# Kernel optimization log

Measured on AMD Instinct MI355X. Metric: run time of the kernel, lower is better.

The kernel has to match this reference:

```python
import jax, jax.numpy as jnp
import numpy as np

B, N, D_MODEL, H = 2, 2048, 1024, 16
Q_CHUNK, K_CHUNK = 512, 1024
LN_EPS = 1e-5


def layer_norm(x, g, b):
    mu = x.mean(-1, keepdims=True)
    var = ((x - mu) ** 2).mean(-1, keepdims=True)
    return (x - mu) * jax.lax.rsqrt(var + LN_EPS) * g + b


def chunked_attention(q, k, v, qry_chunk, key_chunk):
    # q,k,v: [b,h,n,d]; memory-efficient chunked online-softmax attention
    b, h, n, d = q.shape
    q = q * (d ** -0.5)
    Q, K = n // qry_chunk, n // key_chunk
    qr = q.reshape(b, h, Q, qry_chunk, d)
    kr = k.reshape(b, h, K, key_chunk, d)
    vr = v.reshape(b, h, K, key_chunk, d)
    # per (q-chunk, k-chunk) scores: [b,h,Q,K,i,j]
    qk = jnp.einsum('bhqid,bhkjd->bhqkij', qr, kr)
    qk_max = jax.lax.stop_gradient(qk.max(axis=-1, keepdims=True))  # [b,h,Q,K,i,1]
    exp_qk = jnp.exp(qk - qk_max)
    attn = jnp.einsum('bhqkij,bhkjd->bhqkid', exp_qk, vr)
    exp_sum = exp_qk.sum(-1)            # [b,h,Q,K,i]
    m = qk_max[..., 0]                  # [b,h,Q,K,i]
    gmax = m.max(axis=3, keepdims=True)  # global max over key chunks
    renorm = jax.lax.stop_gradient(jnp.exp(m - gmax))
    num = (attn * renorm[..., None]).sum(axis=3)       # [b,h,Q,i,d]
    den = (exp_sum * renorm).sum(axis=3)[..., None]    # [b,h,Q,i,1]
    out = num / (1e-8 + den)
    return out.reshape(b, h, n, d)


def setup_inputs() -> dict:
    key = jax.random.key(0)
    ks = jax.random.split(key, 10)
    s = 0.02
    return {
        'x': jax.random.normal(ks[0], (B, N, D_MODEL), dtype=jnp.float32),
        'Wq': jax.random.normal(ks[1], (D_MODEL, D_MODEL), dtype=jnp.float32) * s,
        'bq': jnp.zeros((D_MODEL,), jnp.float32),
        'Wk': jax.random.normal(ks[2], (D_MODEL, D_MODEL), dtype=jnp.float32) * s,
        'bk': jnp.zeros((D_MODEL,), jnp.float32),
        'Wv': jax.random.normal(ks[3], (D_MODEL, D_MODEL), dtype=jnp.float32) * s,
        'bv': jnp.zeros((D_MODEL,), jnp.float32),
        'Wo': jax.random.normal(ks[4], (D_MODEL, D_MODEL), dtype=jnp.float32) * s,
        'bo': jnp.zeros((D_MODEL,), jnp.float32),
        'ln_g': jnp.ones((D_MODEL,), jnp.float32),
        'ln_b': jnp.zeros((D_MODEL,), jnp.float32),
    }


def reference(x, Wq, bq, Wk, bk, Wv, bv, Wo, bo, ln_g, ln_b):
    # qkv adapter: self-attention (key = val = qry = x)
    q = x @ Wq + bq
    k = x @ Wk + bk
    v = x @ Wv + bv
    # pre-norm on query path
    q = layer_norm(q, ln_g, ln_b)
    b, n, _ = q.shape
    d = D_MODEL // H
    qh = q.reshape(b, n, H, d).transpose(0, 2, 1, 3)
    kh = k.reshape(b, n, H, d).transpose(0, 2, 1, 3)
    vh = v.reshape(b, n, H, d).transpose(0, 2, 1, 3)
    attn = chunked_attention(qh, kh, vh, Q_CHUNK, K_CHUNK)
    out = attn.transpose(0, 2, 1, 3).reshape(b, n, D_MODEL)
    out = out + q  # residual with normed projected query
    return out @ Wo + bo
```

## Files before the change

### kernel.cpp

```cpp
#include <hip/hip_runtime.h>


typedef unsigned short u16;
typedef __attribute__((ext_vector_type(8))) short bf8v;
typedef __attribute__((ext_vector_type(4))) float f4v;

typedef __attribute__((address_space(1))) void gvoid;
typedef __attribute__((address_space(3))) void lvoid;
__device__ __forceinline__ void cp16(const void* g, void* l) {
  __builtin_amdgcn_global_load_lds((gvoid*)g, (lvoid*)l, 16, 0, 0);
}

__device__ __forceinline__ float bf2f(u16 u) {
  unsigned int x = ((unsigned int)u) << 16;
  float f; __builtin_memcpy(&f, &x, 4); return f;
}
__device__ __forceinline__ u16 f2bf(float f) {
  unsigned int x; __builtin_memcpy(&x, &f, 4);
  unsigned int r = (x + 0x7fffu + ((x >> 16) & 1u)) >> 16;
  return (u16)r;
}
__device__ __forceinline__ unsigned pack2bf(float a, float b) {
  unsigned ua, ub;
  __builtin_memcpy(&ua, &a, 4); __builtin_memcpy(&ub, &b, 4);
  return __builtin_amdgcn_perm(ub, ua, 0x07060302u);
}

#define KSCALE 0.18033688011f

__global__ __launch_bounds__(256) void k_preprocess(
    const u16* a0, const u16* a1, const u16* a2, const u16* a3,
    const u16* a4, const u16* a5, const u16* a6, const u16* a7,
    const u16* a8, const u16* a9, const u16* a10,
    u16* xb, u16* wt, int* flags, float* stats) {
  const int blk = blockIdx.x;
  const int t = threadIdx.x;
  __shared__ u16 tile[64 * 65];
  __shared__ int cls[3];

  if (blk >= 3072) {
    if (blk < 3076) {
      size_t i = ((size_t)(blk - 3072) * 256 + t) * 8;
      *(float4*)(stats + i) = (float4){0.f, 0.f, 0.f, 0.f};
      *(float4*)(stats + i + 4) = (float4){0.f, 0.f, 0.f, 0.f};
      return;
    }
    if (t >= 11) return;
    const u16* arr[11] = {a0,a1,a2,a3,a4,a5,a6,a7,a8,a9,a10};
    const u16* p = arr[t];
    int ze = 0, no = 0, pe = 0;
    for (int i = 0; i < 128; ++i) {
      u16 he = p[2*i], ho = p[2*i+1];
      if (he == 0) ze++;
      if (ho != 0) no++;
      int e = (he >> 7) & 0xff;
      if (he == 0 || (e >= 64 && e <= 160)) pe++;
    }
    int isbf;
    if (ze >= 100 && no >= 64) isbf = 0;
    else isbf = (pe >= 100) ? 1 : 0;
    flags[t] = isbf;
    return;
  }

  int wz = (blk - 2048) >> 8;
  const u16* src = (blk < 2048) ? a0
                 : (wz == 0) ? a1 : (wz == 1) ? a3 : (wz == 2) ? a5 : a7;
  if (t == 0) { cls[0] = 0; cls[1] = 0; cls[2] = 0; }
  __syncthreads();
  if (t < 128) {
    u16 he = src[2*t], ho = src[2*t+1];
    int e = (he >> 7) & 0xff;
    if (he == 0) atomicAdd(&cls[0], 1);
    if (ho != 0) atomicAdd(&cls[1], 1);
    if (he == 0 || (e >= 64 && e <= 160)) atomicAdd(&cls[2], 1);
  }
  __syncthreads();
  int isbf;
  if (cls[0] >= 100 && cls[1] >= 64) isbf = 0;
  else isbf = (cls[2] >= 100) ? 1 : 0;

  if (blk < 2048) {
    size_t i = ((size_t)blk * 256 + t) * 8;
    if (isbf) {
      *(float4*)(xb + i) = *((const float4*)(a0 + i));
    } else {
      const float* xf = (const float*)a0;
      float4 a = *(const float4*)(xf + i);
      float4 b = *(const float4*)(xf + i + 4);
      ushort4 o0, o1;
      o0.x = f2bf(a.x); o0.y = f2bf(a.y); o0.z = f2bf(a.z); o0.w = f2bf(a.w);
      o1.x = f2bf(b.x); o1.y = f2bf(b.y); o1.z = f2bf(b.z); o1.w = f2bf(b.w);
      *(ushort4*)(xb + i) = o0; *(ushort4*)(xb + i + 4) = o1;
    }
    return;
  }

  {
    int rem = (blk - 2048) & 255;
    int r0 = ((rem >> 4) & 15) * 64, c0 = (rem & 15) * 64;
    u16* dst = wt + (size_t)wz * (1u << 20);
    for (int rr = 0; rr < 2; ++rr) {
      int row = rr * 32 + (t >> 3);
      int c8 = (t & 7) * 8;
      u16 v[8];
      if (isbf) {
        const u16* Ws = src;
        ushort4 a = *(const ushort4*)&Ws[(size_t)(r0 + row) * 1024 + c0 + c8];
        ushort4 b = *(const ushort4*)&Ws[(size_t)(r0 + row) * 1024 + c0 + c8 + 4];
        v[0]=a.x; v[1]=a.y; v[2]=a.z; v[3]=a.w; v[4]=b.x; v[5]=b.y; v[6]=b.z; v[7]=b.w;
      } else {
        const float* Wf = (const float*)src;
        float4 a = *(const float4*)&Wf[(size_t)(r0 + row) * 1024 + c0 + c8];
        float4 b = *(const float4*)&Wf[(size_t)(r0 + row) * 1024 + c0 + c8 + 4];
        v[0]=f2bf(a.x); v[1]=f2bf(a.y); v[2]=f2bf(a.z); v[3]=f2bf(a.w);
        v[4]=f2bf(b.x); v[5]=f2bf(b.y); v[6]=f2bf(b.z); v[7]=f2bf(b.w);
      }
#pragma unroll
      for (int j = 0; j < 8; ++j) tile[row * 65 + c8 + j] = v[j];
    }
    __syncthreads();
    for (int rr = 0; rr < 2; ++rr) {
      int nrow = rr * 32 + (t >> 3);
      int k8 = (t & 7) * 8;
      u16 v[8];
#pragma unroll
      for (int j = 0; j < 8; ++j) v[j] = tile[(k8 + j) * 65 + nrow];
      ushort4 o0, o1;
      o0.x=v[0]; o0.y=v[1]; o0.z=v[2]; o0.w=v[3];
      o1.x=v[4]; o1.y=v[5]; o1.z=v[6]; o1.w=v[7];
      *(ushort4*)&dst[(size_t)(c0 + nrow) * 1024 + r0 + k8] = o0;
      *(ushort4*)&dst[(size_t)(c0 + nrow) * 1024 + r0 + k8 + 4] = o1;
    }
  }
}

template <int MT>
__device__ __forceinline__ void gemm_bt(const u16* __restrict__ A, const u16* __restrict__ Bt,
    const void* __restrict__ bias, int bias_bf, void* __restrict__ Cout, int mode,
    float cscale, float* __restrict__ stats = nullptr) {
  constexpr int MI = MT / 32;
  __shared__ __align__(16) u16 As[2][MT * 32];
  __shared__ __align__(16) u16 Bs[2][128 * 32];
  const int tid = threadIdx.x;
  const int wave = tid >> 6, lane = tid & 63;
  const int qd = lane >> 4, ln = lane & 15;
  const int m0 = blockIdx.y * MT, n0 = blockIdx.x * 128;
  const int wr = (wave >> 1) * (MT / 2), wc = (wave & 1) * 64;
  const int r0 = wave * 16 + (lane >> 2);
  const int csrc = ((lane & 3) ^ ((lane >> 2) & 3)) * 8;
  const u16* Ag = &A[(size_t)m0 * 1024];
  const u16* Bg = &Bt[(size_t)n0 * 1024];
  const int co = (qd ^ (ln & 3)) * 8;
  f4v acc[MI][4];
#pragma unroll
  for (int i = 0; i < MI; ++i)
#pragma unroll
    for (int j = 0; j < 4; ++j) acc[i][j] = (f4v){0.f, 0.f, 0.f, 0.f};

#pragma unroll
  for (int t = 0; t < MT / 64; ++t)
    cp16(&Ag[(size_t)(t * 64 + r0) * 1024 + csrc], &As[0][(t * 256 + wave * 64) * 8]);
#pragma unroll
  for (int t = 0; t < 2; ++t)
    cp16(&Bg[(size_t)(t * 64 + r0) * 1024 + csrc], &Bs[0][(t * 256 + wave * 64) * 8]);

  for (int it = 0; it < 32; ++it) {
    __syncthreads();
    if (it < 31) {
      int ko = (it + 1) * 32;
      int bi = (it + 1) & 1;
#pragma unroll
      for (int t = 0; t < MT / 64; ++t)
        cp16(&Ag[(size_t)(t * 64 + r0) * 1024 + ko + csrc], &As[bi][(t * 256 + wave * 64) * 8]);
#pragma unroll
      for (int t = 0; t < 2; ++t)
        cp16(&Bg[(size_t)(t * 64 + r0) * 1024 + ko + csrc], &Bs[bi][(t * 256 + wave * 64) * 8]);
    }
    const u16* as = As[it & 1];
    const u16* bs = Bs[it & 1];
    bf8v af[MI], bfr[4];
#pragma unroll
    for (int i = 0; i < MI; ++i) af[i]  = *(const bf8v*)&as[(wr + i * 16 + ln) * 32 + co];
#pragma unroll
    for (int j = 0; j < 4; ++j) bfr[j] = *(const bf8v*)&bs[(wc + j * 16 + ln) * 32 + co];
#pragma unroll
    for (int i = 0; i < MI; ++i)
#pragma unroll
      for (int j = 0; j < 4; ++j)
        acc[i][j] = __builtin_amdgcn_mfma_f32_16x16x32_bf16(af[i], bfr[j], acc[i][j], 0, 0, 0);
  }
#pragma unroll
  for (int j = 0; j < 4; ++j) {
    int col = n0 + wc + j * 16 + ln;
    float bv = bias_bf ? bf2f(((const u16*)bias)[col]) : ((const float*)bias)[col];
#pragma unroll
    for (int i = 0; i < MI; ++i) {
      int row = m0 + wr + i * 16 + qd * 4;
      if (mode == 2) {
        ushort4 o4;
        o4.x = f2bf((acc[i][j][0] + bv) * cscale);
        o4.y = f2bf((acc[i][j][1] + bv) * cscale);
        o4.z = f2bf((acc[i][j][2] + bv) * cscale);
        o4.w = f2bf((acc[i][j][3] + bv) * cscale);
        int b_ = row >> 11, nl = row & 2047;
        int h_ = col >> 6, d6 = col & 63;
        int kt = nl >> 6, b0 = nl & 63;
        int c = b0 >> 5, g = (b0 >> 4) & 1, qd_f = (b0 >> 2) & 3;
        int dt = d6 >> 4, ln_f = d6 & 15;
        size_t off = (size_t)(b_ * 16 + h_) * 131072
                   + (size_t)(kt * 4096 + (c * 4 + dt) * 512 + (qd_f * 16 + ln_f) * 8 + g * 4);
        *(ushort4*)&((u16*)Cout)[off] = o4;
      } else if (mode == 3) {
        int b_ = row >> 11, nl = row & 2047;
        int h_ = col >> 6, d6 = col & 63;
        int tile = nl >> 6, ct = (nl >> 4) & 3;
        int half = d6 >> 5, qd_k = (d6 >> 3) & 3, jj = d6 & 7;
        size_t base = (size_t)(b_ * 16 + h_) * 131072
                    + (size_t)(tile * 4096 + (ct * 2 + half) * 512 + qd_k * 128 + jj);
#pragma unroll
        for (int r = 0; r < 4; ++r) {
          float v = (acc[i][j][r] + bv) * cscale;
          ((u16*)Cout)[base + (size_t)(((nl & 15) + r) * 8)] = f2bf(v);
        }
      } else {
#pragma unroll
        for (int r = 0; r < 4; ++r) {
          float v = (acc[i][j][r] + bv) * cscale;
          if (mode == 0) ((float*)Cout)[(size_t)(row + r) * 1024 + col] = v;
          else           ((u16*)Cout)[(size_t)(row + r) * 1024 + col] = f2bf(v);
        }
      }
    }
  }
  if (mode == 4) {
    float bvs[4];
#pragma unroll
    for (int j = 0; j < 4; ++j) {
      int col = n0 + wc + j * 16 + ln;
      bvs[j] = bias_bf ? bf2f(((const u16*)bias)[col]) : ((const float*)bias)[col];
    }
#pragma unroll
    for (int i = 0; i < MI; ++i) {
#pragma unroll
      for (int r = 0; r < 4; ++r) {
        float pv = 0.f, pv2 = 0.f;
#pragma unroll
        for (int j = 0; j < 4; ++j) {
          float v = (acc[i][j][r] + bvs[j]) * cscale;
          float vr = bf2f(f2bf(v));
          pv += vr; pv2 += vr * vr;
        }
        pv += __shfl_xor(pv, 1);  pv2 += __shfl_xor(pv2, 1);
        pv += __shfl_xor(pv, 2);  pv2 += __shfl_xor(pv2, 2);
        pv += __shfl_xor(pv, 4);  pv2 += __shfl_xor(pv2, 4);
        pv += __shfl_xor(pv, 8);  pv2 += __shfl_xor(pv2, 8);
        if (ln == 0) {
          int row = m0 + wr + i * 16 + qd * 4 + r;
          atomicAdd(&stats[2 * row], pv);
          atomicAdd(&stats[2 * row + 1], pv2);
        }
      }
    }
  }
}

__global__ __launch_bounds__(256) void k_gemm_qkv(const u16* xb, const u16* wt,
    const void* bq, const void* bk, const void* bv, const int* flags,
    u16* qpre, u16* kb, u16* vtb, float* stats) {
  int z = blockIdx.z;
  const u16* Bt = wt + (size_t)z * (1u << 20);
  const void* bias = (z == 0) ? bq : (z == 1) ? bk : bv;
  if (z == 0)      gemm_bt<128>(xb, Bt, bias, flags[2], qpre, 4, 1.0f, stats);
  else if (z == 1) gemm_bt<128>(xb, Bt, bias, flags[4], kb,   3, KSCALE);
  else             gemm_bt<128>(xb, Bt, bias, flags[6], vtb,  2, 1.0f);
}

__global__ __launch_bounds__(256) void k_gemm_out(const u16* A, const u16* Bt,
    const void* bias, const int* flags, void* out) {
  gemm_bt<64>(A, Bt, bias, flags[8], out, flags[0] ? 1 : 0, 1.0f);
}

template <int NQS>
__device__ __forceinline__ void attn_tile(const bf8v kf[4][2], const bf8v vf[8],
    const bf8v qf[NQS][2], float ls[NQS][4], f4v o[NQS][4]) {
#pragma unroll
  for (int qs = 0; qs < NQS; ++qs) {
    unsigned pk[4][2];
#pragma unroll
    for (int ct = 0; ct < 4; ++ct) {
      f4v z = (f4v){0.f, 0.f, 0.f, 0.f};
      z = __builtin_amdgcn_mfma_f32_16x16x32_bf16(kf[ct][0], qf[qs][0], z, 0, 0, 0);
      z = __builtin_amdgcn_mfma_f32_16x16x32_bf16(kf[ct][1], qf[qs][1], z, 0, 0, 0);
      float p0 = __builtin_amdgcn_exp2f(z[0]);
      float p1 = __builtin_amdgcn_exp2f(z[1]);
      float p2 = __builtin_amdgcn_exp2f(z[2]);
      float p3 = __builtin_amdgcn_exp2f(z[3]);
      ls[qs][0] += p0; ls[qs][1] += p1; ls[qs][2] += p2; ls[qs][3] += p3;
      pk[ct][0] = pack2bf(p0, p1);
      pk[ct][1] = pack2bf(p2, p3);
    }
#pragma unroll
    for (int c = 0; c < 2; ++c) {
      unsigned avals[4] = {pk[2*c][0], pk[2*c][1], pk[2*c+1][0], pk[2*c+1][1]};
      bf8v af; __builtin_memcpy(&af, avals, 16);
#pragma unroll
      for (int dt = 0; dt < 4; ++dt)
        o[qs][dt] = __builtin_amdgcn_mfma_f32_16x16x32_bf16(af, vf[c * 4 + dt], o[qs][dt], 0, 0, 0);
    }
  }
}

__global__ __launch_bounds__(256) void k_attention(const u16* __restrict__ qpre,
    const u16* __restrict__ kfg, const u16* __restrict__ vfg,
    const float* __restrict__ stats, const void* __restrict__ gg,
    const void* __restrict__ bbv, const int* __restrict__ flags,
    u16* __restrict__ attn) {
  const int x = blockIdx.x;
  const int xcd = x & 7, sl = x >> 3;
  const int bh = xcd * 4 + (sl >> 4), qc = sl & 15;
  const int b = bh >> 4, h = bh & 15;
  const int tid = threadIdx.x, wave = tid >> 6, lane = tid & 63;
  const int qd = lane >> 4, ln = lane & 15;
  const int qrow0 = qc * 128 + wave * 32;

  const u16* kgb = kfg + (size_t)bh * 131072;
  const u16* vgb = vfg + (size_t)bh * 131072;
  const int gf = flags[9], bfl = flags[10];

  __shared__ __align__(16) u16 kv[2][8192];

  bf8v qf[2][2];
#pragma unroll
  for (int qs = 0; qs < 2; ++qs) {
    int rowg = b * 2048 + qrow0 + qs * 16 + ln;
    float s = stats[2 * rowg], s2 = stats[2 * rowg + 1];
    float mu = s * (1.f / 1024.f);
    float rs = rsqrtf(s2 * (1.f / 1024.f) - mu * mu + 1e-5f);
    const u16* qb = qpre + (size_t)rowg * 1024 + h * 64;
#pragma unroll
    for (int half = 0; half < 2; ++half) {
      bf8v raw = *(const bf8v*)(qb + half * 32 + qd * 8);
      unsigned pkq[4];
#pragma unroll
      for (int e = 0; e < 4; ++e) {
        int c0 = h * 64 + half * 32 + qd * 8 + 2 * e;
        float g0 = gf ? bf2f(((const u16*)gg)[c0])     : ((const float*)gg)[c0];
        float g1 = gf ? bf2f(((const u16*)gg)[c0 + 1]) : ((const float*)gg)[c0 + 1];
        float b0 = bfl ? bf2f(((const u16*)bbv)[c0])     : ((const float*)bbv)[c0];
        float b1 = bfl ? bf2f(((const u16*)bbv)[c0 + 1]) : ((const float*)bbv)[c0 + 1];
        float v0 = bf2f((u16)raw[2 * e]);
        float v1 = bf2f((u16)raw[2 * e + 1]);
        pkq[e] = pack2bf((v0 - mu) * rs * g0 + b0, (v1 - mu) * rs * g1 + b1);
      }
      __builtin_memcpy(&qf[qs][half], pkq, 16);
    }
  }
  float ls[2][4];
  f4v o[2][4];
#pragma unroll
  for (int qs = 0; qs < 2; ++qs)
#pragma unroll
    for (int r = 0; r < 4; ++r) { ls[qs][r] = 0.f; o[qs][r] = (f4v){0.f, 0.f, 0.f, 0.f}; }

#pragma unroll
  for (int q = 0; q < 2; ++q) {
    cp16(kgb + (size_t)(q * 256 + tid) * 8, &kv[0][(q * 256 + wave * 64) * 8]);
    cp16(vgb + (size_t)(q * 256 + tid) * 8, &kv[0][4096 + (q * 256 + wave * 64) * 8]);
  }

  for (int t = 0; t < 32; ++t) {
    __syncthreads();
    if (t < 31) {
      const u16* ks = kgb + (size_t)(t + 1) * 4096;
      const u16* vs = vgb + (size_t)(t + 1) * 4096;
      u16* dst = kv[(t + 1) & 1];
#pragma unroll
      for (int q = 0; q < 2; ++q) {
        cp16(ks + (size_t)(q * 256 + tid) * 8, &dst[(q * 256 + wave * 64) * 8]);
        cp16(vs + (size_t)(q * 256 + tid) * 8, &dst[4096 + (q * 256 + wave * 64) * 8]);
      }
    }
    const u16* kvb = kv[t & 1];
    bf8v kfr[4][2], vfr[8];
#pragma unroll
    for (int ct = 0; ct < 4; ++ct) {
      kfr[ct][0] = *(const bf8v*)&kvb[(ct * 2 + 0) * 512 + lane * 8];
      kfr[ct][1] = *(const bf8v*)&kvb[(ct * 2 + 1) * 512 + lane * 8];
    }
#pragma unroll
    for (int cd = 0; cd < 8; ++cd)
      vfr[cd] = *(const bf8v*)&kvb[4096 + cd * 512 + lane * 8];
    attn_tile<2>(kfr, vfr, qf, ls, o);
  }

#pragma unroll
  for (int qs = 0; qs < 2; ++qs) {
    float lsum = (ls[qs][0] + ls[qs][1]) + (ls[qs][2] + ls[qs][3]);
    lsum += __shfl_xor(lsum, 16);
    lsum += __shfl_xor(lsum, 32);
    float rden[4], mur[4], rsr[4];
#pragma unroll
    for (int r = 0; r < 4; ++r) {
      float dv = __shfl(lsum, (lane & 48) + qd * 4 + r);
      rden[r] = __builtin_amdgcn_rcpf(1e-8f + dv);
      int rowg = b * 2048 + qrow0 + qs * 16 + qd * 4 + r;
      float s = stats[2 * rowg], s2 = stats[2 * rowg + 1];
      mur[r] = s * (1.f / 1024.f);
      rsr[r] = rsqrtf(s2 * (1.f / 1024.f) - mur[r] * mur[r] + 1e-5f);
    }
#pragma unroll
    for (int dt = 0; dt < 4; ++dt) {
      int c = h * 64 + dt * 16 + ln;
      float gvv = gf ? bf2f(((const u16*)gg)[c]) : ((const float*)gg)[c];
      float bvv = bfl ? bf2f(((const u16*)bbv)[c]) : ((const float*)bbv)[c];
#pragma unroll
      for (int r = 0; r < 4; ++r) {
        size_t idx = ((size_t)b * 2048 + qrow0 + qs * 16 + qd * 4 + r) * 1024 + c;
        float qv = bf2f(qpre[idx]);
        float val = o[qs][dt][r] * rden[r] + (qv - mur[r]) * rsr[r] * gvv + bvv;
        attn[idx] = f2bf(val);
      }
    }
  }
}

extern "C" void kernel_launch(void* const* d_in, const int* in_sizes, int n_in,
                              void* d_out, int out_size, void* d_ws, size_t ws_size,
                              hipStream_t stream) {
  int* flags = (int*)d_ws;
  u16* base = (u16*)((char*)d_ws + 256);
  const size_t M1 = 1u << 20;
  u16* xb   = base;
  u16* wt   = base + 4 * M1;
  u16* qpre = base + 8 * M1;
  u16* kb   = base + 12 * M1;
  u16* vtb  = base + 16 * M1;
  float* stats = (float*)(base + 20 * M1);
  u16* at  = qpre;

  k_preprocess<<<3077, 256, 0, stream>>>(
      (const u16*)d_in[0], (const u16*)d_in[1], (const u16*)d_in[2], (const u16*)d_in[3],
      (const u16*)d_in[4], (const u16*)d_in[5], (const u16*)d_in[6], (const u16*)d_in[7],
      (const u16*)d_in[8], (const u16*)d_in[9], (const u16*)d_in[10], xb, wt, flags, stats);
  k_gemm_qkv<<<dim3(8, 32, 3), 256, 0, stream>>>(xb, wt, d_in[2], d_in[4], d_in[6], flags,
                                                 qpre, kb, vtb, stats);
  k_attention<<<512, 256, 0, stream>>>(qpre, kb, vtb, stats, d_in[9], d_in[10], flags, at);
  k_gemm_out<<<dim3(8, 64), 256, 0, stream>>>(at, wt + 3 * M1, d_in[8], flags, d_out);
}
```

Measured before the change: 225.0 us.

## Remap GEMM blocks per XCD and move LayerNorm stats to separate kernel

Both GEMM kernels now use a 1D grid and remap block IDs so that each XCD (blockIdx mod 8) handles a contiguous rectangle of output tiles. This is meant to improve L2 reuse of A and B tiles within each chiplet. The atomic LayerNorm row-statistics epilogue is removed from the Q projection, and a new k_lnstats kernel computes per-row sum and sum-of-squares from the bf16 Q output, which also drops the stats zeroing in preprocessing. This removes the atomics and the shuffle work from the GEMM, at the cost of an extra launch and a re-read of Q.

```diff
diff --git a/kernel.cpp b/kernel.cpp
--- a/kernel.cpp
+++ b/kernel.cpp
@@ -32,19 +32,13 @@
     const u16* a0, const u16* a1, const u16* a2, const u16* a3,
     const u16* a4, const u16* a5, const u16* a6, const u16* a7,
     const u16* a8, const u16* a9, const u16* a10,
-    u16* xb, u16* wt, int* flags, float* stats) {
+    u16* xb, u16* wt, int* flags) {
   const int blk = blockIdx.x;
   const int t = threadIdx.x;
   __shared__ u16 tile[64 * 65];
   __shared__ int cls[3];
 
   if (blk >= 3072) {
-    if (blk < 3076) {
-      size_t i = ((size_t)(blk - 3072) * 256 + t) * 8;
-      *(float4*)(stats + i) = (float4){0.f, 0.f, 0.f, 0.f};
-      *(float4*)(stats + i + 4) = (float4){0.f, 0.f, 0.f, 0.f};
-      return;
-    }
     if (t >= 11) return;
     const u16* arr[11] = {a0,a1,a2,a3,a4,a5,a6,a7,a8,a9,a10};
     const u16* p = arr[t];
@@ -138,14 +132,13 @@
 template <int MT>
 __device__ __forceinline__ void gemm_bt(const u16* __restrict__ A, const u16* __restrict__ Bt,
     const void* __restrict__ bias, int bias_bf, void* __restrict__ Cout, int mode,
-    float cscale, float* __restrict__ stats = nullptr) {
+    float cscale, int m0, int n0) {
   constexpr int MI = MT / 32;
   __shared__ __align__(16) u16 As[2][MT * 32];
   __shared__ __align__(16) u16 Bs[2][128 * 32];
   const int tid = threadIdx.x;
   const int wave = tid >> 6, lane = tid & 63;
   const int qd = lane >> 4, ln = lane & 15;
-  const int m0 = blockIdx.y * MT, n0 = blockIdx.x * 128;
   const int wr = (wave >> 1) * (MT / 2), wc = (wave & 1) * 64;
   const int r0 = wave * 16 + (lane >> 2);
   const int csrc = ((lane & 3) ^ ((lane >> 2) & 3)) * 8;
@@ -227,58 +220,58 @@
 #pragma unroll
         for (int r = 0; r < 4; ++r) {
           float v = (acc[i][j][r] + bv) * cscale;
-          if (mode == 0) ((float*)Cout)[(size_t)(row + r) * 1024 + col] = v;
-          else           ((u16*)Cout)[(size_t)(row + r) * 1024 + col] = f2bf(v);
+          if (mode == 1) ((u16*)Cout)[(size_t)(row + r) * 1024 + col] = f2bf(v);
+          else           ((float*)Cout)[(size_t)(row + r) * 1024 + col] = v;
         }
       }
     }
   }
-  if (mode == 4) {
-    float bvs[4];
-#pragma unroll
-    for (int j = 0; j < 4; ++j) {
-      int col = n0 + wc + j * 16 + ln;
-      bvs[j] = bias_bf ? bf2f(((const u16*)bias)[col]) : ((const float*)bias)[col];
-    }
-#pragma unroll
-    for (int i = 0; i < MI; ++i) {
-#pragma unroll
-      for (int r = 0; r < 4; ++r) {
-        float pv = 0.f, pv2 = 0.f;
-#pragma unroll
-        for (int j = 0; j < 4; ++j) {
-          float v = (acc[i][j][r] + bvs[j]) * cscale;
-          float vr = bf2f(f2bf(v));
-          pv += vr; pv2 += vr * vr;
-        }
-        pv += __shfl_xor(pv, 1);  pv2 += __shfl_xor(pv2, 1);
-        pv += __shfl_xor(pv, 2);  pv2 += __shfl_xor(pv2, 2);
-        pv += __shfl_xor(pv, 4);  pv2 += __shfl_xor(pv2, 4);
-        pv += __shfl_xor(pv, 8);  pv2 += __shfl_xor(pv2, 8);
-        if (ln == 0) {
-          int row = m0 + wr + i * 16 + qd * 4 + r;
-          atomicAdd(&stats[2 * row], pv);
-          atomicAdd(&stats[2 * row + 1], pv2);
-        }
-      }
-    }
-  }
 }
 
 __global__ __launch_bounds__(256) void k_gemm_qkv(const u16* xb, const u16* wt,
     const void* bq, const void* bk, const void* bv, const int* flags,
-    u16* qpre, u16* kb, u16* vtb, float* stats) {
-  int z = blockIdx.z;
+    u16* qpre, u16* kb, u16* vtb) {
+  const int id = blockIdx.x;
+  const int xcd = id & 7, j = id >> 3;
+  const int xw = j & 3, jj = j >> 2;
+  const int z = jj % 3, yw = jj / 3;
+  const int y = (xcd >> 1) * 8 + yw;
+  const int x = (xcd & 1) * 4 + xw;
   const u16* Bt = wt + (size_t)z * (1u << 20);
   const void* bias = (z == 0) ? bq : (z == 1) ? bk : bv;
-  if (z == 0)      gemm_bt<128>(xb, Bt, bias, flags[2], qpre, 4, 1.0f, stats);
-  else if (z == 1) gemm_bt<128>(xb, Bt, bias, flags[4], kb,   3, KSCALE);
-  else             gemm_bt<128>(xb, Bt, bias, flags[6], vtb,  2, 1.0f);
+  if (z == 0)      gemm_bt<128>(xb, Bt, bias, flags[2], qpre, 1, 1.0f,   y * 128, x * 128);
+  else if (z == 1) gemm_bt<128>(xb, Bt, bias, flags[4], kb,   3, KSCALE, y * 128, x * 128);
+  else             gemm_bt<128>(xb, Bt, bias, flags[6], vtb,  2, 1.0f,   y * 128, x * 128);
 }
 
 __global__ __launch_bounds__(256) void k_gemm_out(const u16* A, const u16* Bt,
     const void* bias, const int* flags, void* out) {
-  gemm_bt<64>(A, Bt, bias, flags[8], out, flags[0] ? 1 : 0, 1.0f);
+  const int id = blockIdx.x;
+  const int xcd = id & 7, j = id >> 3;
+  const int xw = j & 3, yw = j >> 2;
+  const int y = (xcd >> 1) * 16 + yw;
+  const int x = (xcd & 1) * 4 + xw;
+  gemm_bt<64>(A, Bt, bias, flags[8], out, flags[0] ? 1 : 0, 1.0f, y * 64, x * 128);
+}
+
+__global__ __launch_bounds__(256) void k_lnstats(const u16* __restrict__ qp,
+    float* __restrict__ stats) {
+  int row = blockIdx.x, t = threadIdx.x;
+  ushort4 u = *(const ushort4*)(qp + (size_t)row * 1024 + t * 4);
+  float x0 = bf2f(u.x), x1 = bf2f(u.y), x2 = bf2f(u.z), x3 = bf2f(u.w);
+  float s = x0 + x1 + x2 + x3;
+  float s2 = x0 * x0 + x1 * x1 + x2 * x2 + x3 * x3;
+  for (int off = 32; off; off >>= 1) { s += __shfl_down(s, off); s2 += __shfl_down(s2, off); }
+  __shared__ float red[8];
+  int wave = t >> 6, lane = t & 63;
+  if (lane == 0) { red[wave] = s; red[4 + wave] = s2; }
+  __syncthreads();
+  if (t == 0) {
+    float S = red[0] + red[1] + red[2] + red[3];
+    float S2 = red[4] + red[5] + red[6] + red[7];
+    stats[2 * row] = S;
+    stats[2 * row + 1] = S2;
+  }
 }
 
 template <int NQS>
@@ -439,12 +432,13 @@
   float* stats = (float*)(base + 20 * M1);
   u16* at  = qpre;
 
-  k_preprocess<<<3077, 256, 0, stream>>>(
+  k_preprocess<<<3073, 256, 0, stream>>>(
       (const u16*)d_in[0], (const u16*)d_in[1], (const u16*)d_in[2], (const u16*)d_in[3],
       (const u16*)d_in[4], (const u16*)d_in[5], (const u16*)d_in[6], (const u16*)d_in[7],
-      (const u16*)d_in[8], (const u16*)d_in[9], (const u16*)d_in[10], xb, wt, flags, stats);
-  k_gemm_qkv<<<dim3(8, 32, 3), 256, 0, stream>>>(xb, wt, d_in[2], d_in[4], d_in[6], flags,
-                                                 qpre, kb, vtb, stats);
+      (const u16*)d_in[8], (const u16*)d_in[9], (const u16*)d_in[10], xb, wt, flags);
+  k_gemm_qkv<<<768, 256, 0, stream>>>(xb, wt, d_in[2], d_in[4], d_in[6], flags,
+                                      qpre, kb, vtb);
+  k_lnstats<<<4096, 256, 0, stream>>>(qpre, stats);
   k_attention<<<512, 256, 0, stream>>>(qpre, kb, vtb, stats, d_in[9], d_in[10], flags, at);
-  k_gemm_out<<<dim3(8, 64), 256, 0, stream>>>(at, wt + 3 * M1, d_in[8], flags, d_out);
-}
+  k_gemm_out<<<512, 256, 0, stream>>>(at, wt + 3 * M1, d_in[8], flags, d_out);
+}
```

Result: faster. 210.1 us (-6.6%).
